# Performance work log

Measured on AMD Instinct MI355X. Metric: run time of the kernel, lower is better.

The kernel has to match this reference:

```python
import jax, jax.numpy as jnp
import numpy as np

POS_LEN = 32  # S = POS_LEN**2 = 1024
NUM_F = 16    # fourier features -> input dim 8*16 = 128
HIDDEN = 256
T = 32        # gab_num_templates


def _offsets(pos_len):
    S = pos_len * pos_len
    s_idx = jnp.arange(S)
    s_r = s_idx // pos_len
    s_c = s_idx % pos_len
    dr = (s_r[:, None] - s_r[None, :]).astype(jnp.float32)
    dc = (s_c[:, None] - s_c[None, :]).astype(jnp.float32)
    return dr, dc


def setup_inputs() -> dict:
    key = jax.random.key(0)
    k1, k2, k3, k4 = jax.random.split(key, 4)
    # learnable freqs: exp(linspace(log(1), log(1/50)))
    freqs = jnp.exp(jnp.linspace(jnp.log(1.0), jnp.log(1.0 / 50.0), NUM_F)).astype(jnp.float32)
    fin = 8 * NUM_F
    W1 = jax.random.normal(k1, (HIDDEN, fin), dtype=jnp.float32) * (1.0 / np.sqrt(fin))
    b1 = jax.random.normal(k2, (HIDDEN,), dtype=jnp.float32) * 0.01
    W2 = jax.random.normal(k3, (T, HIDDEN), dtype=jnp.float32) * (1.0 / np.sqrt(HIDDEN))
    b2 = jax.random.normal(k4, (T,), dtype=jnp.float32) * 0.01
    dr, dc = _offsets(POS_LEN)
    return {"seq_len": POS_LEN * POS_LEN, "freqs": freqs, "W1": W1, "b1": b1,
            "W2": W2, "b2": b2, "dr": dr, "dc": dc}


def _fourier_features(dr, dc, freqs):
    # dr, dc: (S, S); freqs: (F,) -> (S, S, 8F)
    f = freqs[None, None, :]
    a = dr[..., None] * f
    b = dc[..., None] * f
    p = (dr + dc)[..., None] * f
    m = (dr - dc)[..., None] * f
    return jnp.concatenate([jnp.sin(a), jnp.cos(a), jnp.sin(b), jnp.cos(b),
                            jnp.sin(p), jnp.cos(p), jnp.sin(m), jnp.cos(m)], axis=-1)


def reference(seq_len, freqs, W1, b1, W2, b2, dr, dc):
    dr_s = dr[:seq_len, :seq_len]
    dc_s = dc[:seq_len, :seq_len]
    feats = _fourier_features(dr_s, dc_s, freqs)          # (S, S, 8F)
    h = jax.nn.silu(jnp.einsum('ijf,hf->ijh', feats, W1) + b1)  # (S, S, H)
    out = jnp.einsum('ijh,th->ijt', h, W2) + b2            # (S, S, T)
    return out * (1.0 / jnp.sqrt(jnp.float32(T)))
```

## Files before the change

### kernel.cpp

```cpp
#include <hip/hip_runtime.h>
#include <math.h>

#define NUM_F   16
#define FIN     (8 * NUM_F)
#define HIDDEN  256
#define TOUT    32
#define NOFF    63
#define NSUM    125
#define NPAIRS_TBL (NOFF * NOFF)
#define PROWS   (NOFF + NOFF + NSUM + NSUM)

__global__ __launch_bounds__(256) void gab_ptab_kernel(
    const float* __restrict__ freqs, const float* __restrict__ W1,
    float* __restrict__ P)
{
    __shared__ float fv_all[8][32];

    const int b = blockIdx.x;
    int g, c;
    if (b < 8)       { g = 0; c = b; }
    else if (b < 16) { g = 1; c = b - 8; }
    else if (b < 32) { g = 2; c = b - 16; }
    else             { g = 3; c = b - 32; }
    const int nrows   = (g < 2) ? NOFF : NSUM;
    const int rowbase = (g == 0) ? 0 : (g == 1) ? NOFF
                      : (g == 2) ? 2 * NOFF : 2 * NOFF + NSUM;
    const int voff    = (g < 2) ? 31 : 62;

    const int t = threadIdx.x;

    {
        const int r  = t >> 5;
        const int e  = t & 31;
        const int gr = c * 8 + r;
        if (gr < nrows) {
            const float arg = (float)(gr - voff) * freqs[e & 15];
            fv_all[r][e] = (e < 16) ? sinf(arg) : cosf(arg);
        }
    }

    float4 w1c[8];
    {
        const float4* w4 = (const float4*)(W1 + t * FIN + g * 32);
        #pragma unroll
        for (int k = 0; k < 8; ++k) w1c[k] = w4[k];
    }
    __syncthreads();

    #pragma unroll
    for (int r = 0; r < 8; ++r) {
        const int gr = c * 8 + r;
        if (gr >= nrows) break;
        const float4* f4 = (const float4*)fv_all[r];
        float a0 = 0.f, a1 = 0.f, a2 = 0.f, a3 = 0.f;
        #pragma unroll
        for (int k = 0; k < 8; k += 2) {
            const float4 fa = f4[k], fb = f4[k + 1];
            a0 = fmaf(w1c[k].x,     fa.x, a0); a1 = fmaf(w1c[k].y,     fa.y, a1);
            a2 = fmaf(w1c[k].z,     fa.z, a2); a3 = fmaf(w1c[k].w,     fa.w, a3);
            a0 = fmaf(w1c[k + 1].x, fb.x, a0); a1 = fmaf(w1c[k + 1].y, fb.y, a1);
            a2 = fmaf(w1c[k + 1].z, fb.z, a2); a3 = fmaf(w1c[k + 1].w, fb.w, a3);
        }
        P[(rowbase + gr) * HIDDEN + t] = (a0 + a1) + (a2 + a3);
    }
}

__global__ __launch_bounds__(256) void gab_table_kernel(
    const float* __restrict__ P, const float* __restrict__ b1,
    const float* __restrict__ W2, const float* __restrict__ b2,
    float* __restrict__ table)
{
    const int pair = blockIdx.x * 4 + (threadIdx.x >> 6);
    if (pair >= NPAIRS_TBL) return;
    const int l = threadIdx.x & 63;

    const int ia = pair / NOFF;
    const int ib = pair % NOFF;
    const int ip = ia + ib;
    const int im = ia - ib + 62;

    const float4* __restrict__ P4 = (const float4*)P;
    const float4 pa = P4[(0 * NOFF              + ia) * 64 + l];
    const float4 pb = P4[(1 * NOFF              + ib) * 64 + l];
    const float4 pp = P4[(2 * NOFF              + ip) * 64 + l];
    const float4 pm = P4[((2 * NOFF + NSUM)     + im) * 64 + l];
    const float4 bb = ((const float4*)b1)[l];

    float h0 = pa.x + pb.x + pp.x + pm.x + bb.x;
    float h1 = pa.y + pb.y + pp.y + pm.y + bb.y;
    float h2 = pa.z + pb.z + pp.z + pm.z + bb.z;
    float h3 = pa.w + pb.w + pp.w + pm.w + bb.w;
    h0 = h0 / (1.0f + expf(-h0));
    h1 = h1 / (1.0f + expf(-h1));
    h2 = h2 / (1.0f + expf(-h2));
    h3 = h3 / (1.0f + expf(-h3));

    float acc[32];
    const float4* __restrict__ W24 = (const float4*)W2;
    #pragma unroll
    for (int o = 0; o < 32; ++o) {
        const float4 w = W24[o * 64 + l];
        acc[o] = fmaf(w.x, h0, fmaf(w.y, h1, fmaf(w.z, h2, w.w * h3)));
    }

    #pragma unroll
    for (int i = 0; i < 16; ++i) {
        const float keep = (l & 1) ? acc[i + 16] : acc[i];
        const float send = (l & 1) ? acc[i] : acc[i + 16];
        acc[i] = keep + __shfl_xor(send, 1);
    }
    #pragma unroll
    for (int i = 0; i < 8; ++i) {
        const float keep = (l & 2) ? acc[i + 8] : acc[i];
        const float send = (l & 2) ? acc[i] : acc[i + 8];
        acc[i] = keep + __shfl_xor(send, 2);
    }
    #pragma unroll
    for (int i = 0; i < 4; ++i) {
        const float keep = (l & 4) ? acc[i + 4] : acc[i];
        const float send = (l & 4) ? acc[i] : acc[i + 4];
        acc[i] = keep + __shfl_xor(send, 4);
    }
    #pragma unroll
    for (int i = 0; i < 2; ++i) {
        const float keep = (l & 8) ? acc[i + 2] : acc[i];
        const float send = (l & 8) ? acc[i] : acc[i + 2];
        acc[i] = keep + __shfl_xor(send, 8);
    }
    {
        const float keep = (l & 16) ? acc[1] : acc[0];
        const float send = (l & 16) ? acc[0] : acc[1];
        acc[0] = keep + __shfl_xor(send, 16);
    }
    const float tot = acc[0] + __shfl_xor(acc[0], 32);

    if (l < 32) {
        const int o = ((l & 1) << 4) | ((l & 2) << 2) | (l & 4)
                    | ((l & 8) >> 2) | ((l & 16) >> 4);
        table[pair * TOUT + o] = (tot + b2[o]) * 0.17677669529663687f;
    }
}

__global__ __launch_bounds__(256, 2) void gab_table_fallback(
    const float* __restrict__ freqs,
    const float* __restrict__ W1, const float* __restrict__ b1,
    const float* __restrict__ W2, const float* __restrict__ b2,
    float* __restrict__ table)
{
    __shared__ float feats[FIN];
    __shared__ float hbuf2[HIDDEN];
    __shared__ float part2[4][33];

    const int t = threadIdx.x;
    const int o = t & 31;
    const int c = t >> 5;

    float4 w1r[32];
    {
        const float4* w1v = (const float4*)(W1 + t * FIN);
        #pragma unroll
        for (int k = 0; k < 32; ++k) w1r[k] = w1v[k];
    }
    float4 w2r[8];
    {
        const float4* w2v = (const float4*)(W2 + o * HIDDEN + c * 32);
        #pragma unroll
        for (int k = 0; k < 8; ++k) w2r[k] = w2v[k];
    }
    const float b1t = b1[t];
    const float b2o = b2[o];
    const float myfreq = (t < FIN) ? freqs[t & 15] : 0.0f;

    for (int pp = 0; pp < 8; ++pp) {
        const int pair = blockIdx.x * 8 + pp;
        if (pair >= NPAIRS_TBL) break;
        const float dr = (float)(pair / NOFF - (NOFF / 2));
        const float dc = (float)(pair % NOFF - (NOFF / 2));

        if (t < FIN) {
            const int g = t >> 4;
            float bse;
            switch (g >> 1) {
                case 0:  bse = dr;      break;
                case 1:  bse = dc;      break;
                case 2:  bse = dr + dc; break;
                default: bse = dr - dc; break;
            }
            const float arg = bse * myfreq;
            feats[t] = (g & 1) ? cosf(arg) : sinf(arg);
        }
        __syncthreads();

        float a0 = 0.f, a1 = 0.f, a2 = 0.f, a3 = 0.f;
        const float4* f4 = (const float4*)feats;
        #pragma unroll
        for (int k = 0; k < 32; k += 2) {
            float4 fa = f4[k], fb = f4[k + 1];
            a0 = fmaf(w1r[k].x,     fa.x, a0); a1 = fmaf(w1r[k].y,     fa.y, a1);
            a2 = fmaf(w1r[k].z,     fa.z, a2); a3 = fmaf(w1r[k].w,     fa.w, a3);
            a0 = fmaf(w1r[k + 1].x, fb.x, a0); a1 = fmaf(w1r[k + 1].y, fb.y, a1);
            a2 = fmaf(w1r[k + 1].z, fb.z, a2); a3 = fmaf(w1r[k + 1].w, fb.w, a3);
        }
        const float pre = (a0 + a1) + (a2 + a3) + b1t;
        hbuf2[t] = pre / (1.0f + expf(-pre));
        __syncthreads();

        float s0 = 0.f, s1 = 0.f, s2 = 0.f, s3 = 0.f;
        const float4* h4 = (const float4*)(hbuf2 + c * 32);
        #pragma unroll
        for (int k = 0; k < 8; k += 2) {
            float4 ha = h4[k], hb = h4[k + 1];
            s0 = fmaf(w2r[k].x,     ha.x, s0); s1 = fmaf(w2r[k].y,     ha.y, s1);
            s2 = fmaf(w2r[k].z,     ha.z, s2); s3 = fmaf(w2r[k].w,     ha.w, s3);
            s0 = fmaf(w2r[k + 1].x, hb.x, s0); s1 = fmaf(w2r[k + 1].y, hb.y, s1);
            s2 = fmaf(w2r[k + 1].z, hb.z, s2); s3 = fmaf(w2r[k + 1].w, hb.w, s3);
        }
        float s = (s0 + s1) + (s2 + s3);
        s += __shfl_xor(s, 32);
        if ((t & 63) < 32) part2[t >> 6][o] = s;
        __syncthreads();
        if (t < TOUT) {
            const float r = part2[0][t] + part2[1][t] + part2[2][t] + part2[3][t] + b2o;
            table[pair * TOUT + t] = r * 0.17677669529663687f;
        }
        __syncthreads();
    }
}

__global__ __launch_bounds__(256) void gab_gather_kernel(
    const float* __restrict__ table,
    float4* __restrict__ out, int npairs)
{
    const int total = npairs * 8;
    const int stride = gridDim.x * blockDim.x;
    const float4* __restrict__ tbl4 = (const float4*)table;

    for (int idx = blockIdx.x * blockDim.x + threadIdx.x; idx < total; idx += stride) {
        const int p = idx >> 3;
        const int l = idx & 7;
        const int i = p >> 10;
        const int j = p & 1023;
        const int ir = (i >> 5) - (j >> 5) + (NOFF / 2);
        const int ic = (i & 31) - (j & 31) + (NOFF / 2);
        out[idx] = tbl4[(ir * NOFF + ic) * (TOUT / 4) + l];
    }
}

extern "C" void kernel_launch(void* const* d_in, const int* in_sizes, int n_in,
                              void* d_out, int out_size, void* d_ws, size_t ws_size,
                              hipStream_t stream) {
    const float* freqs = (const float*)d_in[1];
    const float* W1    = (const float*)d_in[2];
    const float* b1    = (const float*)d_in[3];
    const float* W2    = (const float*)d_in[4];
    const float* b2    = (const float*)d_in[5];
    float* out = (float*)d_out;

    const int npairs = in_sizes[6];

    const size_t TBL_B = (size_t)NPAIRS_TBL * TOUT * 4;
    const size_t P_B   = (size_t)PROWS * HIDDEN * 4;
    float* table = (float*)d_ws;

    if (ws_size >= TBL_B + P_B) {
        float* P = (float*)((char*)d_ws + TBL_B);
        gab_ptab_kernel <<<48, 256, 0, stream>>>(freqs, W1, P);
        gab_table_kernel<<<(NPAIRS_TBL + 3) / 4, 256, 0, stream>>>(P, b1, W2, b2, table);
    } else {
        gab_table_fallback<<<(NPAIRS_TBL + 7) / 8, 256, 0, stream>>>(freqs, W1, b1, W2, b2, table);
    }

    gab_gather_kernel<<<2048, 256, 0, stream>>>(table, (float4*)out, npairs);
}
```

Before: 40.16 us.

## Fuse three kernels into one cooperative persistent kernel with grid syncs

Merges the projection-table, pair-table and gather stages into one cooperative kernel that uses grid-wide syncs between phases, so two kernel launches and their gaps disappear. The projection stage now gives each block one row and reads W1 straight from global memory instead of caching a slice in registers. It adds occupancy and device-attribute queries on the host every call, and grid.sync is costly. The gather phase now runs on fewer blocks than before, which may cut memory parallelism for the large output write. The fallback path is restructured and the old no-workspace fallback is removed.

Result: slower. 153.1 us (+281.3%).

```diff
diff --git a/kernel.cpp b/kernel.cpp
--- a/kernel.cpp
+++ b/kernel.cpp
@@ -1,5 +1,8 @@
 #include <hip/hip_runtime.h>
+#include <hip/hip_cooperative_groups.h>
 #include <math.h>
+
+namespace cg = cooperative_groups;
 
 #define NUM_F   16
 #define FIN     (8 * NUM_F)
@@ -10,59 +13,169 @@
 #define NPAIRS_TBL (NOFF * NOFF)
 #define PROWS   (NOFF + NOFF + NSUM + NSUM)
 
+__global__ __launch_bounds__(256, 2) void gab_mega_kernel(
+    const float* __restrict__ freqs,
+    const float* __restrict__ W1, const float* __restrict__ b1,
+    const float* __restrict__ W2, const float* __restrict__ b2,
+    float* __restrict__ P, float* __restrict__ table,
+    float4* __restrict__ out, int npairs)
+{
+    cg::grid_group grid = cg::this_grid();
+    const int t  = threadIdx.x;
+    const int b  = blockIdx.x;
+    const int nb = gridDim.x;
+
+    {
+        __shared__ float fv[32];
+        for (int rho = b; rho < PROWS; rho += nb) {
+            int grp, val;
+            if (rho < NOFF)                 { grp = 0; val = rho - 31; }
+            else if (rho < 2 * NOFF)        { grp = 1; val = rho - NOFF - 31; }
+            else if (rho < 2 * NOFF + NSUM) { grp = 2; val = rho - 2 * NOFF - 62; }
+            else                            { grp = 3; val = rho - 2 * NOFF - NSUM - 62; }
+
+            if (t < 32) {
+                const float arg = (float)val * freqs[t & 15];
+                fv[t] = (t < 16) ? sinf(arg) : cosf(arg);
+            }
+            __syncthreads();
+
+            const float4* __restrict__ w4 = (const float4*)(W1 + t * FIN + grp * 32);
+            const float4* f4 = (const float4*)fv;
+            float a0 = 0.f, a1 = 0.f, a2 = 0.f, a3 = 0.f;
+            #pragma unroll
+            for (int k = 0; k < 8; k += 2) {
+                const float4 wa = w4[k], wb = w4[k + 1];
+                const float4 fa = f4[k], fb = f4[k + 1];
+                a0 = fmaf(wa.x, fa.x, a0); a1 = fmaf(wa.y, fa.y, a1);
+                a2 = fmaf(wa.z, fa.z, a2); a3 = fmaf(wa.w, fa.w, a3);
+                a0 = fmaf(wb.x, fb.x, a0); a1 = fmaf(wb.y, fb.y, a1);
+                a2 = fmaf(wb.z, fb.z, a2); a3 = fmaf(wb.w, fb.w, a3);
+            }
+            P[rho * HIDDEN + t] = (a0 + a1) + (a2 + a3);
+            __syncthreads();
+        }
+    }
+    __threadfence();
+    grid.sync();
+
+    {
+        const int l = t & 63;
+        for (int pair = b * 4 + (t >> 6); pair < NPAIRS_TBL; pair += nb * 4) {
+            const int ia = pair / NOFF;
+            const int ib = pair % NOFF;
+            const int ip = ia + ib;
+            const int im = ia - ib + 62;
+
+            const float4* __restrict__ P4 = (const float4*)P;
+            const float4 pa = P4[(0 * NOFF          + ia) * 64 + l];
+            const float4 pb = P4[(1 * NOFF          + ib) * 64 + l];
+            const float4 pp = P4[(2 * NOFF          + ip) * 64 + l];
+            const float4 pm = P4[((2 * NOFF + NSUM) + im) * 64 + l];
+            const float4 bb = ((const float4*)b1)[l];
+
+            float h0 = pa.x + pb.x + pp.x + pm.x + bb.x;
+            float h1 = pa.y + pb.y + pp.y + pm.y + bb.y;
+            float h2 = pa.z + pb.z + pp.z + pm.z + bb.z;
+            float h3 = pa.w + pb.w + pp.w + pm.w + bb.w;
+            h0 = h0 / (1.0f + expf(-h0));
+            h1 = h1 / (1.0f + expf(-h1));
+            h2 = h2 / (1.0f + expf(-h2));
+            h3 = h3 / (1.0f + expf(-h3));
+
+            float acc[32];
+            const float4* __restrict__ W24 = (const float4*)W2;
+            #pragma unroll
+            for (int o = 0; o < 32; ++o) {
+                const float4 w = W24[o * 64 + l];
+                acc[o] = fmaf(w.x, h0, fmaf(w.y, h1, fmaf(w.z, h2, w.w * h3)));
+            }
+            #pragma unroll
+            for (int i = 0; i < 16; ++i) {
+                const float keep = (l & 1) ? acc[i + 16] : acc[i];
+                const float send = (l & 1) ? acc[i] : acc[i + 16];
+                acc[i] = keep + __shfl_xor(send, 1);
+            }
+            #pragma unroll
+            for (int i = 0; i < 8; ++i) {
+                const float keep = (l & 2) ? acc[i + 8] : acc[i];
+                const float send = (l & 2) ? acc[i] : acc[i + 8];
+                acc[i] = keep + __shfl_xor(send, 2);
+            }
+            #pragma unroll
+            for (int i = 0; i < 4; ++i) {
+                const float keep = (l & 4) ? acc[i + 4] : acc[i];
+                const float send = (l & 4) ? acc[i] : acc[i + 4];
+                acc[i] = keep + __shfl_xor(send, 4);
+            }
+            #pragma unroll
+            for (int i = 0; i < 2; ++i) {
+                const float keep = (l & 8) ? acc[i + 2] : acc[i];
+                const float send = (l & 8) ? acc[i] : acc[i + 2];
+                acc[i] = keep + __shfl_xor(send, 8);
+            }
+            {
+                const float keep = (l & 16) ? acc[1] : acc[0];
+                const float send = (l & 16) ? acc[0] : acc[1];
+                acc[0] = keep + __shfl_xor(send, 16);
+            }
+            const float tot = acc[0] + __shfl_xor(acc[0], 32);
+
+            if (l < 32) {
+                const int o = ((l & 1) << 4) | ((l & 2) << 2) | (l & 4)
+                            | ((l & 8) >> 2) | ((l & 16) >> 4);
+                table[pair * TOUT + o] = (tot + b2[o]) * 0.17677669529663687f;
+            }
+        }
+    }
+    __threadfence();
+    grid.sync();
+
+    {
+        const int total = npairs * 8;
+        const float4* __restrict__ tbl4 = (const float4*)table;
+        for (int idx = b * 256 + t; idx < total; idx += nb * 256) {
+            const int p  = idx >> 3;
+            const int l4 = idx & 7;
+            const int i  = p >> 10;
+            const int j  = p & 1023;
+            const int ir = (i >> 5) - (j >> 5) + (NOFF / 2);
+            const int ic = (i & 31) - (j & 31) + (NOFF / 2);
+            out[idx] = tbl4[(ir * NOFF + ic) * (TOUT / 4) + l4];
+        }
+    }
+}
+
 __global__ __launch_bounds__(256) void gab_ptab_kernel(
     const float* __restrict__ freqs, const float* __restrict__ W1,
     float* __restrict__ P)
 {
-    __shared__ float fv_all[8][32];
-
-    const int b = blockIdx.x;
-    int g, c;
-    if (b < 8)       { g = 0; c = b; }
-    else if (b < 16) { g = 1; c = b - 8; }
-    else if (b < 32) { g = 2; c = b - 16; }
-    else             { g = 3; c = b - 32; }
-    const int nrows   = (g < 2) ? NOFF : NSUM;
-    const int rowbase = (g == 0) ? 0 : (g == 1) ? NOFF
-                      : (g == 2) ? 2 * NOFF : 2 * NOFF + NSUM;
-    const int voff    = (g < 2) ? 31 : 62;
-
+    __shared__ float fv[32];
+    const int rho = blockIdx.x;
+    int grp, val;
+    if (rho < NOFF)                 { grp = 0; val = rho - 31; }
+    else if (rho < 2 * NOFF)        { grp = 1; val = rho - NOFF - 31; }
+    else if (rho < 2 * NOFF + NSUM) { grp = 2; val = rho - 2 * NOFF - 62; }
+    else                            { grp = 3; val = rho - 2 * NOFF - NSUM - 62; }
     const int t = threadIdx.x;
-
-    {
-        const int r  = t >> 5;
-        const int e  = t & 31;
-        const int gr = c * 8 + r;
-        if (gr < nrows) {
-            const float arg = (float)(gr - voff) * freqs[e & 15];
-            fv_all[r][e] = (e < 16) ? sinf(arg) : cosf(arg);
-        }
-    }
-
-    float4 w1c[8];
-    {
-        const float4* w4 = (const float4*)(W1 + t * FIN + g * 32);
-        #pragma unroll
-        for (int k = 0; k < 8; ++k) w1c[k] = w4[k];
+    if (t < 32) {
+        const float arg = (float)val * freqs[t & 15];
+        fv[t] = (t < 16) ? sinf(arg) : cosf(arg);
     }
     __syncthreads();
-
-    #pragma unroll
-    for (int r = 0; r < 8; ++r) {
-        const int gr = c * 8 + r;
-        if (gr >= nrows) break;
-        const float4* f4 = (const float4*)fv_all[r];
-        float a0 = 0.f, a1 = 0.f, a2 = 0.f, a3 = 0.f;
-        #pragma unroll
-        for (int k = 0; k < 8; k += 2) {
-            const float4 fa = f4[k], fb = f4[k + 1];
-            a0 = fmaf(w1c[k].x,     fa.x, a0); a1 = fmaf(w1c[k].y,     fa.y, a1);
-            a2 = fmaf(w1c[k].z,     fa.z, a2); a3 = fmaf(w1c[k].w,     fa.w, a3);
-            a0 = fmaf(w1c[k + 1].x, fb.x, a0); a1 = fmaf(w1c[k + 1].y, fb.y, a1);
-            a2 = fmaf(w1c[k + 1].z, fb.z, a2); a3 = fmaf(w1c[k + 1].w, fb.w, a3);
-        }
-        P[(rowbase + gr) * HIDDEN + t] = (a0 + a1) + (a2 + a3);
-    }
+    const float4* __restrict__ w4 = (const float4*)(W1 + t * FIN + grp * 32);
+    const float4* f4 = (const float4*)fv;
+    float a0 = 0.f, a1 = 0.f, a2 = 0.f, a3 = 0.f;
+    #pragma unroll
+    for (int k = 0; k < 8; k += 2) {
+        const float4 wa = w4[k], wb = w4[k + 1];
+        const float4 fa = f4[k], fb = f4[k + 1];
+        a0 = fmaf(wa.x, fa.x, a0); a1 = fmaf(wa.y, fa.y, a1);
+        a2 = fmaf(wa.z, fa.z, a2); a3 = fmaf(wa.w, fa.w, a3);
+        a0 = fmaf(wb.x, fb.x, a0); a1 = fmaf(wb.y, fb.y, a1);
+        a2 = fmaf(wb.z, fb.z, a2); a3 = fmaf(wb.w, fb.w, a3);
+    }
+    P[rho * HIDDEN + t] = (a0 + a1) + (a2 + a3);
 }
 
 __global__ __launch_bounds__(256) void gab_table_kernel(
@@ -73,19 +186,16 @@
     const int pair = blockIdx.x * 4 + (threadIdx.x >> 6);
     if (pair >= NPAIRS_TBL) return;
     const int l = threadIdx.x & 63;
-
     const int ia = pair / NOFF;
     const int ib = pair % NOFF;
     const int ip = ia + ib;
     const int im = ia - ib + 62;
-
     const float4* __restrict__ P4 = (const float4*)P;
-    const float4 pa = P4[(0 * NOFF              + ia) * 64 + l];
-    const float4 pb = P4[(1 * NOFF              + ib) * 64 + l];
-    const float4 pp = P4[(2 * NOFF              + ip) * 64 + l];
-    const float4 pm = P4[((2 * NOFF + NSUM)     + im) * 64 + l];
+    const float4 pa = P4[(0 * NOFF          + ia) * 64 + l];
+    const float4 pb = P4[(1 * NOFF          + ib) * 64 + l];
+    const float4 pp = P4[(2 * NOFF          + ip) * 64 + l];
+    const float4 pm = P4[((2 * NOFF + NSUM) + im) * 64 + l];
     const float4 bb = ((const float4*)b1)[l];
-
     float h0 = pa.x + pb.x + pp.x + pm.x + bb.x;
     float h1 = pa.y + pb.y + pp.y + pm.y + bb.y;
     float h2 = pa.z + pb.z + pp.z + pm.z + bb.z;
@@ -94,7 +204,6 @@
     h1 = h1 / (1.0f + expf(-h1));
     h2 = h2 / (1.0f + expf(-h2));
     h3 = h3 / (1.0f + expf(-h3));
-
     float acc[32];
     const float4* __restrict__ W24 = (const float4*)W2;
     #pragma unroll
@@ -102,7 +211,6 @@
         const float4 w = W24[o * 64 + l];
         acc[o] = fmaf(w.x, h0, fmaf(w.y, h1, fmaf(w.z, h2, w.w * h3)));
     }
-
     #pragma unroll
     for (int i = 0; i < 16; ++i) {
         const float keep = (l & 1) ? acc[i + 16] : acc[i];
@@ -133,97 +241,10 @@
         acc[0] = keep + __shfl_xor(send, 16);
     }
     const float tot = acc[0] + __shfl_xor(acc[0], 32);
-
     if (l < 32) {
         const int o = ((l & 1) << 4) | ((l & 2) << 2) | (l & 4)
                     | ((l & 8) >> 2) | ((l & 16) >> 4);
         table[pair * TOUT + o] = (tot + b2[o]) * 0.17677669529663687f;
-    }
-}
-
-__global__ __launch_bounds__(256, 2) void gab_table_fallback(
-    const float* __restrict__ freqs,
-    const float* __restrict__ W1, const float* __restrict__ b1,
-    const float* __restrict__ W2, const float* __restrict__ b2,
-    float* __restrict__ table)
-{
-    __shared__ float feats[FIN];
-    __shared__ float hbuf2[HIDDEN];
-    __shared__ float part2[4][33];
-
-    const int t = threadIdx.x;
-    const int o = t & 31;
-    const int c = t >> 5;
-
-    float4 w1r[32];
-    {
-        const float4* w1v = (const float4*)(W1 + t * FIN);
-        #pragma unroll
-        for (int k = 0; k < 32; ++k) w1r[k] = w1v[k];
-    }
-    float4 w2r[8];
-    {
-        const float4* w2v = (const float4*)(W2 + o * HIDDEN + c * 32);
-        #pragma unroll
-        for (int k = 0; k < 8; ++k) w2r[k] = w2v[k];
-    }
-    const float b1t = b1[t];
-    const float b2o = b2[o];
-    const float myfreq = (t < FIN) ? freqs[t & 15] : 0.0f;
-
-    for (int pp = 0; pp < 8; ++pp) {
-        const int pair = blockIdx.x * 8 + pp;
-        if (pair >= NPAIRS_TBL) break;
-        const float dr = (float)(pair / NOFF - (NOFF / 2));
-        const float dc = (float)(pair % NOFF - (NOFF / 2));
-
-        if (t < FIN) {
-            const int g = t >> 4;
-            float bse;
-            switch (g >> 1) {
-                case 0:  bse = dr;      break;
-                case 1:  bse = dc;      break;
-                case 2:  bse = dr + dc; break;
-                default: bse = dr - dc; break;
-            }
-            const float arg = bse * myfreq;
-            feats[t] = (g & 1) ? cosf(arg) : sinf(arg);
-        }
-        __syncthreads();
-
-        float a0 = 0.f, a1 = 0.f, a2 = 0.f, a3 = 0.f;
-        const float4* f4 = (const float4*)feats;
-        #pragma unroll
-        for (int k = 0; k < 32; k += 2) {
-            float4 fa = f4[k], fb = f4[k + 1];
-            a0 = fmaf(w1r[k].x,     fa.x, a0); a1 = fmaf(w1r[k].y,     fa.y, a1);
-            a2 = fmaf(w1r[k].z,     fa.z, a2); a3 = fmaf(w1r[k].w,     fa.w, a3);
-            a0 = fmaf(w1r[k + 1].x, fb.x, a0); a1 = fmaf(w1r[k + 1].y, fb.y, a1);
-            a2 = fmaf(w1r[k + 1].z, fb.z, a2); a3 = fmaf(w1r[k + 1].w, fb.w, a3);
-        }
-        const float pre = (a0 + a1) + (a2 + a3) + b1t;
-        hbuf2[t] = pre / (1.0f + expf(-pre));
-        __syncthreads();
-
-        float s0 = 0.f, s1 = 0.f, s2 = 0.f, s3 = 0.f;
-        const float4* h4 = (const float4*)(hbuf2 + c * 32);
-        #pragma unroll
-        for (int k = 0; k < 8; k += 2) {
-            float4 ha = h4[k], hb = h4[k + 1];
-            s0 = fmaf(w2r[k].x,     ha.x, s0); s1 = fmaf(w2r[k].y,     ha.y, s1);
-            s2 = fmaf(w2r[k].z,     ha.z, s2); s3 = fmaf(w2r[k].w,     ha.w, s3);
-            s0 = fmaf(w2r[k + 1].x, hb.x, s0); s1 = fmaf(w2r[k + 1].y, hb.y, s1);
-            s2 = fmaf(w2r[k + 1].z, hb.z, s2); s3 = fmaf(w2r[k + 1].w, hb.w, s3);
-        }
-        float s = (s0 + s1) + (s2 + s3);
-        s += __shfl_xor(s, 32);
-        if ((t & 63) < 32) part2[t >> 6][o] = s;
-        __syncthreads();
-        if (t < TOUT) {
-            const float r = part2[0][t] + part2[1][t] + part2[2][t] + part2[3][t] + b2o;
-            table[pair * TOUT + t] = r * 0.17677669529663687f;
-        }
-        __syncthreads();
     }
 }
 
@@ -234,7 +255,6 @@
     const int total = npairs * 8;
     const int stride = gridDim.x * blockDim.x;
     const float4* __restrict__ tbl4 = (const float4*)table;
-
     for (int idx = blockIdx.x * blockDim.x + threadIdx.x; idx < total; idx += stride) {
         const int p = idx >> 3;
         const int l = idx & 7;
@@ -254,21 +274,44 @@
     const float* b1    = (const float*)d_in[3];
     const float* W2    = (const float*)d_in[4];
     const float* b2    = (const float*)d_in[5];
-    float* out = (float*)d_out;
-
-    const int npairs = in_sizes[6];
+    float4* out = (float4*)d_out;
+
+    int npairs = in_sizes[6];
 
     const size_t TBL_B = (size_t)NPAIRS_TBL * TOUT * 4;
     const size_t P_B   = (size_t)PROWS * HIDDEN * 4;
     float* table = (float*)d_ws;
-
+    float* P     = (float*)((char*)d_ws + TBL_B);
+
+    bool done = false;
     if (ws_size >= TBL_B + P_B) {
-        float* P = (float*)((char*)d_ws + TBL_B);
-        gab_ptab_kernel <<<48, 256, 0, stream>>>(freqs, W1, P);
+        int dev = 0;
+        (void)hipGetDevice(&dev);
+        int coop = 0;
+        (void)hipDeviceGetAttribute(&coop, hipDeviceAttributeCooperativeLaunch, dev);
+        int ncu = 0;
+        (void)hipDeviceGetAttribute(&ncu, hipDeviceAttributeMultiprocessorCount, dev);
+        int maxBlkPerCU = 0;
+        (void)hipOccupancyMaxActiveBlocksPerMultiprocessor(
+            &maxBlkPerCU, (const void*)gab_mega_kernel, 256, 0);
+
+        if (coop && ncu > 0 && maxBlkPerCU > 0) {
+            int grid = maxBlkPerCU * ncu;
+            if (grid > 1024) grid = 1024;
+            void* args[] = {
+                (void*)&freqs, (void*)&W1, (void*)&b1, (void*)&W2, (void*)&b2,
+                (void*)&P, (void*)&table, (void*)&out, (void*)&npairs
+            };
+            hipError_t e = hipLaunchCooperativeKernel(
+                (const void*)gab_mega_kernel, dim3(grid), dim3(256),
+                args, 0, stream);
+            done = (e == hipSuccess);
+        }
+    }
+
+    if (!done) {
+        gab_ptab_kernel <<<PROWS, 256, 0, stream>>>(freqs, W1, P);
         gab_table_kernel<<<(NPAIRS_TBL + 3) / 4, 256, 0, stream>>>(P, b1, W2, b2, table);
-    } else {
-        gab_table_fallback<<<(NPAIRS_TBL + 7) / 8, 256, 0, stream>>>(freqs, W1, b1, W2, b2, table);
-    }
-
-    gab_gather_kernel<<<2048, 256, 0, stream>>>(table, (float4*)out, npairs);
-}
+        gab_gather_kernel<<<2048, 256, 0, stream>>>(table, out, npairs);
+    }
+}
```
